# Kernel optimization log

Measured on AMD Instinct MI355X. Metric: run time of the kernel, lower is better.

## Reference

```python
import jax, jax.numpy as jnp
import numpy as np

B, F, E, V = 16384, 32, 16, 100000
D, S, K = 4, 8, 2            # domains, shared experts, specific experts per domain
I = F * E                    # input_dim = 512
OUT = 16
EPS = 1e-5


def _bn(x):
    # torch BatchNorm1d training mode: biased variance over batch
    m = jnp.mean(x, axis=0)
    v = jnp.var(x, axis=0)
    return (x - m) / jnp.sqrt(v + EPS)


def setup_inputs() -> dict:
    key = jax.random.key(0)
    ks = jax.random.split(key, 24)
    inp = {
        "ids": jax.random.randint(ks[0], (B, F), 0, V),
        "domain_id": jax.random.randint(ks[1], (B,), 0, D),
        "emb_table": jax.random.normal(ks[2], (F, V, E), jnp.float32) * 0.05,
        "domain_weight": jax.random.normal(ks[3], (D, I), jnp.float32) * 0.06,
        "domain_bias": jax.random.uniform(ks[4], (D, I), jnp.float32),
        # shared experts: BN affine + Linear(I->16)
        "sh_gamma": jnp.ones((S, I), jnp.float32),
        "sh_beta": jnp.zeros((S, I), jnp.float32),
        "sh_W": jax.random.normal(ks[5], (S, I, OUT), jnp.float32) * 0.04,
        "sh_b": jnp.zeros((S, OUT), jnp.float32),
        # domain-specific experts
        "sp_gamma": jnp.ones((D, K, I), jnp.float32),
        "sp_beta": jnp.zeros((D, K, I), jnp.float32),
        "sp_W": jax.random.normal(ks[6], (D, K, I, OUT), jnp.float32) * 0.04,
        "sp_b": jnp.zeros((D, K, OUT), jnp.float32),
        # gate
        "gate_W": jax.random.normal(ks[7], (I, S + K), jnp.float32) * 0.04,
        "gate_b": jnp.zeros((S + K,), jnp.float32),
        # final MLP 16 -> 32 -> 32 -> 1 (Linear+BN+ReLU per hidden layer)
        "mlp_W1": jax.random.normal(ks[8], (OUT, 32), jnp.float32) * 0.25,
        "mlp_b1": jnp.zeros((32,), jnp.float32),
        "mlp_g1": jnp.ones((32,), jnp.float32),
        "mlp_be1": jnp.zeros((32,), jnp.float32),
        "mlp_W2": jax.random.normal(ks[9], (32, 32), jnp.float32) * 0.18,
        "mlp_b2": jnp.zeros((32,), jnp.float32),
        "mlp_g2": jnp.ones((32,), jnp.float32),
        "mlp_be2": jnp.zeros((32,), jnp.float32),
        "mlp_W3": jax.random.normal(ks[10], (32, 1), jnp.float32) * 0.18,
        "mlp_b3": jnp.zeros((1,), jnp.float32),
    }
    return inp


def reference(ids, domain_id, emb_table, domain_weight, domain_bias,
              sh_gamma, sh_beta, sh_W, sh_b,
              sp_gamma, sp_beta, sp_W, sp_b,
              gate_W, gate_b,
              mlp_W1, mlp_b1, mlp_g1, mlp_be1,
              mlp_W2, mlp_b2, mlp_g2, mlp_be2,
              mlp_W3, mlp_b3):
    # embedding lookup: per-field table gather -> [B, F, E] -> [B, I]
    emb = emb_table[jnp.arange(F)[None, :], ids].reshape(B, I)

    # torch.where over domain masks collapses to a gather of per-domain affine
    shared_emb = emb * domain_weight[domain_id] + domain_bias[domain_id]  # [B, I]

    # shared experts: BN stats shared (same input), per-expert affine + linear
    xh = _bn(shared_emb)  # [B, I]
    shared_out = (jnp.einsum('bi,si,sio->bso', xh, sh_gamma, sh_W)
                  + (jnp.einsum('si,sio->so', sh_beta, sh_W) + sh_b)[None])  # [B, S, 16]

    # domain-specific experts run on the FULL batch per domain (dense dispatch)
    dom_in = emb[None] * domain_weight[:, None, :] + domain_bias[:, None, :]  # [D, B, I]
    xh_d = jax.vmap(_bn)(dom_in)  # [D, B, I]
    spec = (jnp.einsum('dbi,dki,dkio->dbko', xh_d, sp_gamma, sp_W)
            + (jnp.einsum('dki,dkio->dko', sp_beta, sp_W) + sp_b)[:, None])  # [D, B, K, 16]
    specific_emb = spec[domain_id, jnp.arange(B)]  # [B, K, 16] (masked select)

    expert_out = jnp.concatenate([shared_out, specific_emb], axis=1)  # [B, S+K, 16]
    gate = jax.nn.softmax(shared_emb @ gate_W + gate_b, axis=-1)       # [B, S+K]
    mix = jnp.sum(expert_out * gate[..., None], axis=1)               # [B, 16]

    h = jax.nn.relu(_bn(mix @ mlp_W1 + mlp_b1) * mlp_g1 + mlp_be1)
    h = jax.nn.relu(_bn(h @ mlp_W2 + mlp_b2) * mlp_g2 + mlp_be2)
    logit = (h @ mlp_W3 + mlp_b3)[:, 0]
    return jax.nn.sigmoid(logit)
```

## Files before the change

kernel.cpp:

```cpp
#include <hip/hip_runtime.h>
#include <hip/hip_bf16.h>

#define B_    16384
#define F_    32
#define E_    16
#define V_    100000
#define D_    4
#define S_    8
#define K_    2
#define I_    512
#define OUT_  16
#define SK_   10
#define C_    192
#define OSTR  193
#define EPS_  1e-5f
#define NG    16

typedef __attribute__((ext_vector_type(4))) float f32x4;
typedef __attribute__((ext_vector_type(8))) short bf16x8;

__device__ __forceinline__ unsigned short f2bf(float x) {
    unsigned u = __float_as_uint(x);
    unsigned r = (u + 0x7fffu + ((u >> 16) & 1u)) >> 16;
    return (unsigned short)r;
}

__global__ __launch_bounds__(512) void k_gather(
    const int* __restrict__ ids, const int* __restrict__ dom,
    const float* __restrict__ tbl, unsigned short* __restrict__ emb,
    float* __restrict__ S1G, float* __restrict__ S2G)
{
    const int t = threadIdx.x;
    const int slot = t & 127;
    const int rsub = t >> 7;
    const int f = slot >> 2;
    const int e0 = (slot & 3) << 2;
    const int rbase = blockIdx.x * 4 + rsub;
    const float* fbase = tbl + (size_t)f * V_ * E_ + e0;

    int idv[8];
#pragma unroll
    for (int it = 0; it < 8; ++it)
        idv[it] = ids[(rbase + it * 2048) * F_ + f];
    float4 v[8];
#pragma unroll
    for (int it = 0; it < 8; ++it)
        v[it] = *(const float4*)(fbase + (size_t)idv[it] * E_);
    int dv[8];
#pragma unroll
    for (int it = 0; it < 8; ++it)
        dv[it] = dom[rbase + it * 2048];

    float sa[4][4], qa[4][4];
#pragma unroll
    for (int d = 0; d < 4; ++d)
#pragma unroll
        for (int c = 0; c < 4; ++c) { sa[d][c] = 0.f; qa[d][c] = 0.f; }

#pragma unroll
    for (int it = 0; it < 8; ++it) {
        const int r = rbase + it * 2048;
        unsigned p0 = (unsigned)f2bf(v[it].x) | ((unsigned)f2bf(v[it].y) << 16);
        unsigned p1 = (unsigned)f2bf(v[it].z) | ((unsigned)f2bf(v[it].w) << 16);
        *(uint2*)(emb + (size_t)r * I_ + slot * 4) = make_uint2(p0, p1);
        const int d = dv[it];
#pragma unroll
        for (int dd = 0; dd < 4; ++dd) {
            const float m = (d == dd) ? 1.f : 0.f;
            sa[dd][0] = fmaf(m, v[it].x, sa[dd][0]); qa[dd][0] = fmaf(m * v[it].x, v[it].x, qa[dd][0]);
            sa[dd][1] = fmaf(m, v[it].y, sa[dd][1]); qa[dd][1] = fmaf(m * v[it].y, v[it].y, qa[dd][1]);
            sa[dd][2] = fmaf(m, v[it].z, sa[dd][2]); qa[dd][2] = fmaf(m * v[it].z, v[it].z, qa[dd][2]);
            sa[dd][3] = fmaf(m, v[it].w, sa[dd][3]); qa[dd][3] = fmaf(m * v[it].w, v[it].w, qa[dd][3]);
        }
    }

    __shared__ float red[2][128][36];
    if (rsub >= 2) {
        float* p = red[rsub - 2][slot];
#pragma unroll
        for (int d = 0; d < 4; ++d)
#pragma unroll
            for (int c = 0; c < 4; ++c) { p[d * 4 + c] = sa[d][c]; p[16 + d * 4 + c] = qa[d][c]; }
    }
    __syncthreads();
    if (rsub < 2) {
        float* p = red[rsub][slot];
#pragma unroll
        for (int d = 0; d < 4; ++d)
#pragma unroll
            for (int c = 0; c < 4; ++c) { sa[d][c] += p[d * 4 + c]; qa[d][c] += p[16 + d * 4 + c]; }
    }
    __syncthreads();
    if (rsub == 1) {
        float* p = red[0][slot];
#pragma unroll
        for (int d = 0; d < 4; ++d)
#pragma unroll
            for (int c = 0; c < 4; ++c) { p[d * 4 + c] = sa[d][c]; p[16 + d * 4 + c] = qa[d][c]; }
    }
    __syncthreads();
    if (rsub == 0) {
        float* p = red[0][slot];
        const int g = blockIdx.x & (NG - 1);
#pragma unroll
        for (int d = 0; d < 4; ++d)
#pragma unroll
            for (int c = 0; c < 4; ++c) {
                atomicAdd(&S1G[(g * 4 + d) * 512 + slot * 4 + c], sa[d][c] + p[d * 4 + c]);
                atomicAdd(&S2G[(g * 4 + d) * 512 + slot * 4 + c], qa[d][c] + p[16 + d * 4 + c]);
            }
    }
}

__global__ __launch_bounds__(256) void k_bucket(
    const int* __restrict__ dom, int* __restrict__ cnt, int* __restrict__ rl)
{
    const int t = threadIdx.x;
    const int r = blockIdx.x * 256 + t;
    const int d = dom[r];
    const int wv = t >> 6;
    const int lane = t & 63;
    __shared__ int wcnt[4][4];
    int myoff = 0;
#pragma unroll
    for (int dd = 0; dd < 4; ++dd) {
        unsigned long long m = __ballot(d == dd);
        if (lane == 0) wcnt[dd][wv] = (int)__popcll(m);
        if (d == dd) myoff = (int)__popcll(m & ((1ull << lane) - 1ull));
    }
    __syncthreads();
    if (t < 4) {
        int c0 = wcnt[t][0], c1 = wcnt[t][1], c2 = wcnt[t][2], c3 = wcnt[t][3];
        int b = atomicAdd(&cnt[t], c0 + c1 + c2 + c3);
        wcnt[t][0] = b; wcnt[t][1] = b + c0; wcnt[t][2] = b + c0 + c1; wcnt[t][3] = b + c0 + c1 + c2;
    }
    __syncthreads();
    rl[d * B_ + wcnt[d][wv] + myoff] = r;
}

__global__ __launch_bounds__(256) void k_stats(
    const float* __restrict__ S1G, const float* __restrict__ S2G, const int* __restrict__ cnt,
    const float* __restrict__ dw, const float* __restrict__ db,
    float* __restrict__ m_, float* __restrict__ dq, float* __restrict__ mu, float* __restrict__ isg)
{
    const int i = blockIdx.x * 256 + threadIdx.x;
    float nd[4], s1v[4], s2v[4], wv[4], bv[4];
#pragma unroll
    for (int d = 0; d < 4; ++d) {
        nd[d] = (float)cnt[d];
        float a = 0.f, b = 0.f;
#pragma unroll
        for (int g = 0; g < NG; ++g) {
            a += S1G[(g * 4 + d) * 512 + i];
            b += S2G[(g * 4 + d) * 512 + i];
        }
        s1v[d] = a; s2v[d] = b;
        wv[d] = dw[d * I_ + i];  bv[d] = db[d * I_ + i];
    }
    const float invB = 1.0f / (float)B_;
    float tot1 = s1v[0] + s1v[1] + s1v[2] + s1v[3];
    float tot2 = s2v[0] + s2v[1] + s2v[2] + s2v[3];
    float m = tot1 * invB;
    float v = fmaxf(tot2 * invB - m * m, 0.f);
    m_[i] = m;
#pragma unroll
    for (int d = 0; d < 4; ++d)
        dq[d * I_ + i] = wv[d] / sqrtf(v * wv[d] * wv[d] + EPS_);
    float ssum = 0.f, ssq = 0.f;
#pragma unroll
    for (int d = 0; d < 4; ++d) {
        ssum += wv[d] * s1v[d] + nd[d] * bv[d];
        ssq  += wv[d] * wv[d] * s2v[d] + 2.f * wv[d] * bv[d] * s1v[d] + nd[d] * bv[d] * bv[d];
    }
    float muv = ssum * invB;
    float var = fmaxf(ssq * invB - muv * muv, 0.f);
    mu[i] = muv;
    isg[i] = 1.f / sqrtf(var + EPS_);
}

__global__ __launch_bounds__(256) void k_fold(
    const float* __restrict__ dw, const float* __restrict__ isg, const float* __restrict__ dq,
    const float* __restrict__ shg, const float* __restrict__ shW,
    const float* __restrict__ spg, const float* __restrict__ spW,
    const float* __restrict__ gW, unsigned short* __restrict__ MB,
    const float* __restrict__ m_, const float* __restrict__ mu,
    const float* __restrict__ db,
    const float* __restrict__ shb_, const float* __restrict__ shb2,
    const float* __restrict__ spb_, const float* __restrict__ spb2,
    const float* __restrict__ gb, float* __restrict__ bias)
{
    const int d = blockIdx.y;
    const int t = threadIdx.x;
    if (blockIdx.x < 192) {
        const int ct = blockIdx.x >> 4, ic = blockIdx.x & 15;
        const int lane = t >> 2, jp = t & 3;
        const int c = ct * 16 + (lane & 15);
        unsigned short hi2[2], lo2[2];
#pragma unroll
        for (int jj = 0; jj < 2; ++jj) {
            const int i = ic * 32 + (lane >> 4) * 8 + jp * 2 + jj;
            float val = 0.f;
            if (c < 128) {
                const int s = c >> 4, o = c & 15;
                val = dw[d * I_ + i] * isg[i] * shg[s * I_ + i] * shW[((size_t)s * I_ + i) * OUT_ + o];
            } else if (c < 160) {
                const int k = (c - 128) >> 4, o = c & 15;
                val = dq[d * I_ + i] * spg[((size_t)(d * K_ + k)) * I_ + i]
                    * spW[(((size_t)(d * K_ + k)) * I_ + i) * OUT_ + o];
            } else if (c < 170) {
                val = dw[d * I_ + i] * gW[i * SK_ + (c - 160)];
            }
            unsigned short h = f2bf(val);
            float hv = __uint_as_float((unsigned)h << 16);
            hi2[jj] = h;
            lo2[jj] = f2bf(val - hv);
        }
        const size_t base = (((size_t)(d * 12 + ct) * 16 + ic) * 2) * 512 + lane * 8 + jp * 2;
        *(ushort2*)(MB + base)       = make_ushort2(hi2[0], hi2[1]);
        *(ushort2*)(MB + base + 512) = make_ushort2(lo2[0], lo2[1]);
        return;
    }
    const int e = blockIdx.x - 192;
    __shared__ float red[256][17];
    float acc[16];
#pragma unroll
    for (int o = 0; o < 16; ++o) acc[o] = 0.f;

    if (e < 8) {
        for (int i = t; i < I_; i += 256) {
            float coef = (db[d * I_ + i] - mu[i]) * isg[i] * shg[e * I_ + i] + shb_[e * I_ + i];
            const float* wp = &shW[((size_t)e * I_ + i) * OUT_];
#pragma unroll
            for (int o = 0; o < 16; ++o) acc[o] += coef * wp[o];
        }
    } else if (e < 10) {
        const int k = e - 8;
        for (int i = t; i < I_; i += 256) {
            float coef = -m_[i] * dq[d * I_ + i] * spg[((size_t)(d * K_ + k)) * I_ + i]
                       + spb_[((size_t)(d * K_ + k)) * I_ + i];
            const float* wp = &spW[(((size_t)(d * K_ + k)) * I_ + i) * OUT_];
#pragma unroll
            for (int o = 0; o < 16; ++o) acc[o] += coef * wp[o];
        }
    } else {
        for (int i = t; i < I_; i += 256) {
            float bb = db[d * I_ + i];
#pragma unroll
            for (int g = 0; g < 10; ++g) acc[g] += bb * gW[i * SK_ + g];
        }
    }
#pragma unroll
    for (int o = 0; o < 16; ++o) red[t][o] = acc[o];
    __syncthreads();
    for (int st = 128; st > 0; st >>= 1) {
        if (t < st) {
#pragma unroll
            for (int o = 0; o < 16; ++o) red[t][o] += red[t + st][o];
        }
        __syncthreads();
    }
    if (t == 0) {
        if (e < 8) {
            for (int o = 0; o < 16; ++o) bias[d * C_ + e * 16 + o] = red[0][o] + shb2[e * 16 + o];
        } else if (e < 10) {
            const int k = e - 8;
            for (int o = 0; o < 16; ++o)
                bias[d * C_ + 128 + k * 16 + o] = red[0][o] + spb2[(d * K_ + k) * 16 + o];
        } else {
            for (int g = 0; g < 10; ++g) bias[d * C_ + 160 + g] = red[0][g] + gb[g];
            for (int c = 170; c < C_; ++c) bias[d * C_ + c] = 0.f;
        }
    }
}

__global__ __launch_bounds__(512) void k_main(
    const unsigned short* __restrict__ emb, const int* __restrict__ rl, const int* __restrict__ cnt,
    const unsigned short* __restrict__ MB, const float* __restrict__ bias,
    const float* __restrict__ W1, const float* __restrict__ b1,
    float* __restrict__ h1g, float* __restrict__ h1s, float* __restrict__ h1q)
{
    const int d = blockIdx.y, tile = blockIdx.x;
    const int base = tile * 32;
    const int rem = cnt[d] - base;
    if (rem <= 0) return;
    const int nn = rem < 32 ? rem : 32;
    const int t = threadIdx.x;

    __shared__ int rid[32];
    __shared__ float smem[32 * OSTR + 32 * 33];
    float* obuf  = smem;
    float* h1buf = smem + 32 * OSTR;

    if (t < 32) rid[t] = rl[d * B_ + base + (t < nn ? t : nn - 1)];
    __syncthreads();

    const int wv = t >> 6, lane = t & 63;
    const int rt = wv & 1, ch = wv >> 1;
    const int l15 = lane & 15, lk = lane >> 4;

    const unsigned short* arow  = emb + (size_t)rid[rt * 16 + l15] * I_ + lk * 8;
    const unsigned short* bbase = MB + (size_t)d * 196608 + (size_t)(ch * 3) * 16384 + lane * 8;

    f32x4 acc[3];
#pragma unroll
    for (int c3 = 0; c3 < 3; ++c3) acc[c3] = (f32x4){0.f, 0.f, 0.f, 0.f};

#pragma unroll 4
    for (int ic = 0; ic < 16; ++ic) {
        const bf16x8 a = *(const bf16x8*)(arow + ic * 32);
#pragma unroll
        for (int c3 = 0; c3 < 3; ++c3) {
            const unsigned short* bp = bbase + (size_t)c3 * 16384 + ic * 1024;
            const bf16x8 bh = *(const bf16x8*)bp;
            const bf16x8 bl = *(const bf16x8*)(bp + 512);
            acc[c3] = __builtin_amdgcn_mfma_f32_16x16x32_bf16(a, bh, acc[c3], 0, 0, 0);
            acc[c3] = __builtin_amdgcn_mfma_f32_16x16x32_bf16(a, bl, acc[c3], 0, 0, 0);
        }
    }

    const float* bd = bias + d * C_;
#pragma unroll
    for (int c3 = 0; c3 < 3; ++c3) {
        const int col = ch * 48 + c3 * 16 + l15;
        const float bv = bd[col];
#pragma unroll
        for (int j = 0; j < 4; ++j) {
            const int row = rt * 16 + lk * 4 + j;
            obuf[row * OSTR + col] = acc[c3][j] + bv;
        }
    }
    __syncthreads();

    if (t < 32) {
        const float* row = &obuf[t * OSTR];
        float g[10];
        float mx = row[160];
#pragma unroll
        for (int e = 1; e < 10; ++e) mx = fmaxf(mx, row[160 + e]);
        float ssum = 0.f;
#pragma unroll
        for (int e = 0; e < 10; ++e) { g[e] = __expf(row[160 + e] - mx); ssum += g[e]; }
        const float inv = 1.f / ssum;
        float mix[16];
#pragma unroll
        for (int o = 0; o < 16; ++o) mix[o] = 0.f;
#pragma unroll
        for (int e = 0; e < 10; ++e) {
#pragma unroll
            for (int o = 0; o < 16; ++o) mix[o] = fmaf(g[e], row[e * 16 + o], mix[o]);
        }
#pragma unroll
        for (int o = 0; o < 16; ++o) mix[o] *= inv;
#pragma unroll
        for (int o2 = 0; o2 < 32; ++o2) {
            float a = b1[o2];
#pragma unroll
            for (int o = 0; o < 16; ++o) a = fmaf(mix[o], W1[o * 32 + o2], a);
            h1buf[t * 33 + o2] = a;
        }
    }
    __syncthreads();
    if (t < 32) {
        float s = 0.f, q = 0.f;
        for (int r = 0; r < nn; ++r) { float v = h1buf[r * 33 + t]; s += v; q += v * v; }
        const int g = (blockIdx.x + blockIdx.y) & (NG - 1);
        atomicAdd(&h1s[g * 32 + t], s); atomicAdd(&h1q[g * 32 + t], q);
    }
#pragma unroll
    for (int k = 0; k < 2; ++k) {
        const int idx = k * 512 + t;
        const int r = idx >> 5, c = idx & 31;
        if (r < nn) h1g[(size_t)rid[r] * 32 + c] = h1buf[r * 33 + c];
    }
}

__global__ __launch_bounds__(256) void k_mlp1(
    const float* __restrict__ h1g, const float* __restrict__ s1, const float* __restrict__ s2,
    const float* __restrict__ g1, const float* __restrict__ be1,
    const float* __restrict__ W2, const float* __restrict__ b2,
    float* __restrict__ h2g, float* __restrict__ h2s, float* __restrict__ h2q)
{
    __shared__ float hb[64 * 33];
    __shared__ float ab[64 * 33];
    __shared__ float w2t[32 * 32];
    __shared__ float scl[32], shf[32];
    const int t = threadIdx.x;
    const size_t rb = (size_t)blockIdx.x * 64;
#pragma unroll
    for (int k = 0; k < 2; ++k) {
        const int w = k * 1024 + t * 4;
        const int r = w >> 5, c = w & 31;
        *(float4*)&hb[r * 33 + c] = *(const float4*)&h1g[rb * 32 + w];
    }
#pragma unroll
    for (int k = 0; k < 4; ++k) {
        const int idx = k * 256 + t;
        const int i = idx >> 5, o = idx & 31;
        w2t[o * 32 + i] = W2[idx];
    }
    if (t < 32) {
        float s = 0.f, q = 0.f;
#pragma unroll
        for (int g = 0; g < NG; ++g) { s += s1[g * 32 + t]; q += s2[g * 32 + t]; }
        const float invB = 1.0f / (float)B_;
        float mn = s * invB;
        float vr = fmaxf(q * invB - mn * mn, 0.f);
        float iv = 1.f / sqrtf(vr + EPS_);
        scl[t] = iv * g1[t]; shf[t] = be1[t] - mn * iv * g1[t];
    }
    __syncthreads();
    const int r = t >> 2, sub = t & 3;
#pragma unroll
    for (int k = 0; k < 8; ++k) {
        const int i = sub * 8 + k;
        float x = hb[r * 33 + i] * scl[i] + shf[i];
        ab[r * 33 + i] = fmaxf(x, 0.f);
    }
    __syncthreads();
    float h2[8];
#pragma unroll
    for (int kk = 0; kk < 8; ++kk) {
        const int o = sub * 8 + kk;
        float acc = b2[o];
#pragma unroll
        for (int i = 0; i < 32; i += 4) {
            const float4 w4 = *(const float4*)&w2t[o * 32 + i];
            acc = fmaf(ab[r * 33 + i], w4.x, acc);
            acc = fmaf(ab[r * 33 + i + 1], w4.y, acc);
            acc = fmaf(ab[r * 33 + i + 2], w4.z, acc);
            acc = fmaf(ab[r * 33 + i + 3], w4.w, acc);
        }
        h2[kk] = acc;
    }
    __syncthreads();
#pragma unroll
    for (int kk = 0; kk < 8; ++kk) hb[r * 33 + sub * 8 + kk] = h2[kk];
    __syncthreads();
    if (t < 32) {
        float s = 0.f, q = 0.f;
        for (int rr = 0; rr < 64; ++rr) { float v = hb[rr * 33 + t]; s += v; q += v * v; }
        const int g = blockIdx.x & (NG - 1);
        atomicAdd(&h2s[g * 32 + t], s); atomicAdd(&h2q[g * 32 + t], q);
    }
#pragma unroll
    for (int k = 0; k < 2; ++k) {
        const int w = k * 1024 + t * 4;
        const int r2 = w >> 5, c = w & 31;
        *(float4*)&h2g[rb * 32 + w] = *(const float4*)&hb[r2 * 33 + c];
    }
}

__global__ __launch_bounds__(256) void k_mlp2(
    const float* __restrict__ h2g, const float* __restrict__ s1, const float* __restrict__ s2,
    const float* __restrict__ g2, const float* __restrict__ be2,
    const float* __restrict__ W3, const float* __restrict__ b3, float* __restrict__ out)
{
    __shared__ float hb[64 * 33];
    __shared__ float scl[32], shf[32], w3s[32];
    const int t = threadIdx.x;
    const size_t rb = (size_t)blockIdx.x * 64;
#pragma unroll
    for (int k = 0; k < 2; ++k) {
        const int w = k * 1024 + t * 4;
        const int r = w >> 5, c = w & 31;
        *(float4*)&hb[r * 33 + c] = *(const float4*)&h2g[rb * 32 + w];
    }
    if (t < 32) {
        float s = 0.f, q = 0.f;
#pragma unroll
        for (int g = 0; g < NG; ++g) { s += s1[g * 32 + t]; q += s2[g * 32 + t]; }
        const float invB = 1.0f / (float)B_;
        float mn = s * invB;
        float vr = fmaxf(q * invB - mn * mn, 0.f);
        float iv = 1.f / sqrtf(vr + EPS_);
        scl[t] = iv * g2[t]; shf[t] = be2[t] - mn * iv * g2[t];
        w3s[t] = W3[t];
    }
    __syncthreads();
    if (t < 64) {
        float acc = b3[0];
#pragma unroll
        for (int i = 0; i < 32; ++i) {
            float x = hb[t * 33 + i] * scl[i] + shf[i];
            x = fmaxf(x, 0.f);
            acc = fmaf(x, w3s[i], acc);
        }
        out[rb + t] = 1.f / (1.f + __expf(-acc));
    }
}

extern "C" void kernel_launch(void* const* d_in, const int* in_sizes, int n_in,
                              void* d_out, int out_size, void* d_ws, size_t ws_size,
                              hipStream_t stream) {
    const int*   ids  = (const int*)d_in[0];
    const int*   dom  = (const int*)d_in[1];
    const float* tbl  = (const float*)d_in[2];
    const float* dw   = (const float*)d_in[3];
    const float* db   = (const float*)d_in[4];
    const float* shg  = (const float*)d_in[5];
    const float* shb_ = (const float*)d_in[6];
    const float* shW  = (const float*)d_in[7];
    const float* shb2 = (const float*)d_in[8];
    const float* spg  = (const float*)d_in[9];
    const float* spb_ = (const float*)d_in[10];
    const float* spW  = (const float*)d_in[11];
    const float* spb2 = (const float*)d_in[12];
    const float* gW   = (const float*)d_in[13];
    const float* gb   = (const float*)d_in[14];
    const float* W1   = (const float*)d_in[15];
    const float* b1   = (const float*)d_in[16];
    const float* g1   = (const float*)d_in[17];
    const float* be1  = (const float*)d_in[18];
    const float* W2   = (const float*)d_in[19];
    const float* b2   = (const float*)d_in[20];
    const float* g2   = (const float*)d_in[21];
    const float* be2  = (const float*)d_in[22];
    const float* W3   = (const float*)d_in[23];
    const float* b3   = (const float*)d_in[24];
    float* out = (float*)d_out;

    float* ws = (float*)d_ws;
    float* S1G  = ws + 0;
    float* S2G  = ws + 32768;
    float* H1S  = ws + 65536;
    float* H1Q  = ws + 66048;
    float* H2S  = ws + 66560;
    float* H2Q  = ws + 67072;
    int*   CNT  = (int*)(ws + 67584);
    float* M0v  = ws + 67600;
    float* DQ   = ws + 68112;
    float* MU   = ws + 70160;
    float* ISG  = ws + 70672;
    float* BIASW= ws + 71184;
    unsigned short* MB = (unsigned short*)(ws + 71952);
    int*   RL   = (int*)(ws + 465168);
    unsigned short* EMB = (unsigned short*)(ws + 530704);
    float* H1G  = ws + 4725008;
    float* H2G  = ws + 5249296;

    hipMemsetAsync(d_ws, 0, 270400, stream);

    k_gather<<<512, 512, 0, stream>>>(ids, dom, tbl, EMB, S1G, S2G);
    k_bucket<<<64, 256, 0, stream>>>(dom, CNT, RL);
    k_stats<<<2, 256, 0, stream>>>(S1G, S2G, CNT, dw, db, M0v, DQ, MU, ISG);
    k_fold<<<dim3(203, 4), 256, 0, stream>>>(dw, ISG, DQ, shg, shW, spg, spW, gW, MB,
                                             M0v, MU, db, shb_, shb2, spb_, spb2, gb, BIASW);
    k_main<<<dim3(512, 4), 512, 0, stream>>>(EMB, RL, CNT, MB, BIASW, W1, b1, H1G, H1S, H1Q);
    k_mlp1<<<256, 256, 0, stream>>>(H1G, H1S, H1Q, g1, be1, W2, b2, H2G, H2S, H2Q);
    k_mlp2<<<256, 256, 0, stream>>>(H2G, H2S, H2Q, g2, be2, W3, b3, out);
}
```

Measured before the change: 383.0 us.

## Fuse domain bucketing into gather, widen stat atomic groups, parallelize gate mix

Domain bucketing (count plus row list) moves into the gather kernel, which removes one launch. Each block counts its 32 rows through shared memory and reserves slots with atomics. The number of atomic partial-sum groups for the embedding stats doubles to 32 to reduce atomic contention, which means a larger memset and a longer reduction loop in k_stats. In k_main, the gate-weighted mix and the W1 projection are spread across all threads through shared buffers, with W1 and b1 staged in LDS, instead of 32 threads doing them serially. Row order inside each domain bucket changes, which alters summation order but not results beyond rounding.

```diff
diff --git a/kernel.cpp b/kernel.cpp
--- a/kernel.cpp
+++ b/kernel.cpp
@@ -14,7 +14,8 @@
 #define C_    192
 #define OSTR  193
 #define EPS_  1e-5f
-#define NG    16
+#define NG    32
+#define NGH   16
 
 typedef __attribute__((ext_vector_type(4))) float f32x4;
 typedef __attribute__((ext_vector_type(8))) short bf16x8;
@@ -28,7 +29,8 @@
 __global__ __launch_bounds__(512) void k_gather(
     const int* __restrict__ ids, const int* __restrict__ dom,
     const float* __restrict__ tbl, unsigned short* __restrict__ emb,
-    float* __restrict__ S1G, float* __restrict__ S2G)
+    float* __restrict__ S1G, float* __restrict__ S2G,
+    int* __restrict__ cnt, int* __restrict__ rl)
 {
     const int t = threadIdx.x;
     const int slot = t & 127;
@@ -38,6 +40,10 @@
     const int rbase = blockIdx.x * 4 + rsub;
     const float* fbase = tbl + (size_t)f * V_ * E_ + e0;
 
+    __shared__ int dombuf[32];
+    __shared__ int dbase[4];
+    __shared__ float red[2][128][36];
+
     int idv[8];
 #pragma unroll
     for (int it = 0; it < 8; ++it)
@@ -50,6 +56,11 @@
 #pragma unroll
     for (int it = 0; it < 8; ++it)
         dv[it] = dom[rbase + it * 2048];
+
+    if (slot == 0) {
+#pragma unroll
+        for (int it = 0; it < 8; ++it) dombuf[rsub * 8 + it] = dv[it];
+    }
 
     float sa[4][4], qa[4][4];
 #pragma unroll
@@ -74,7 +85,6 @@
         }
     }
 
-    __shared__ float red[2][128][36];
     if (rsub >= 2) {
         float* p = red[rsub - 2][slot];
 #pragma unroll
@@ -110,32 +120,20 @@
                 atomicAdd(&S2G[(g * 4 + d) * 512 + slot * 4 + c], qa[d][c] + p[16 + d * 4 + c]);
             }
     }
-}
-
-__global__ __launch_bounds__(256) void k_bucket(
-    const int* __restrict__ dom, int* __restrict__ cnt, int* __restrict__ rl)
-{
-    const int t = threadIdx.x;
-    const int r = blockIdx.x * 256 + t;
-    const int d = dom[r];
-    const int wv = t >> 6;
-    const int lane = t & 63;
-    __shared__ int wcnt[4][4];
-    int myoff = 0;
-#pragma unroll
-    for (int dd = 0; dd < 4; ++dd) {
-        unsigned long long m = __ballot(d == dd);
-        if (lane == 0) wcnt[dd][wv] = (int)__popcll(m);
-        if (d == dd) myoff = (int)__popcll(m & ((1ull << lane) - 1ull));
-    }
-    __syncthreads();
     if (t < 4) {
-        int c0 = wcnt[t][0], c1 = wcnt[t][1], c2 = wcnt[t][2], c3 = wcnt[t][3];
-        int b = atomicAdd(&cnt[t], c0 + c1 + c2 + c3);
-        wcnt[t][0] = b; wcnt[t][1] = b + c0; wcnt[t][2] = b + c0 + c1; wcnt[t][3] = b + c0 + c1 + c2;
-    }
-    __syncthreads();
-    rl[d * B_ + wcnt[d][wv] + myoff] = r;
+        int count = 0;
+#pragma unroll
+        for (int j = 0; j < 32; ++j) count += (dombuf[j] == t);
+        dbase[t] = atomicAdd(&cnt[t], count);
+    }
+    __syncthreads();
+    if (t < 32) {
+        const int d = dombuf[t];
+        int pref = 0;
+        for (int j = 0; j < t; ++j) pref += (dombuf[j] == d);
+        const int row = blockIdx.x * 4 + (t >> 3) + (t & 7) * 2048;
+        rl[d * B_ + dbase[d] + pref] = row;
+    }
 }
 
 __global__ __launch_bounds__(256) void k_stats(
@@ -149,7 +147,6 @@
     for (int d = 0; d < 4; ++d) {
         nd[d] = (float)cnt[d];
         float a = 0.f, b = 0.f;
-#pragma unroll
         for (int g = 0; g < NG; ++g) {
             a += S1G[(g * 4 + d) * 512 + i];
             b += S2G[(g * 4 + d) * 512 + i];
@@ -287,11 +284,16 @@
     const int t = threadIdx.x;
 
     __shared__ int rid[32];
-    __shared__ float smem[32 * OSTR + 32 * 33];
-    float* obuf  = smem;
-    float* h1buf = smem + 32 * OSTR;
+    __shared__ float obuf[32 * OSTR];
+    __shared__ float h1buf[32 * 33];
+    __shared__ float gbuf[32][11];
+    __shared__ float mixbuf[32 * 17];
+    __shared__ float w1s[512];
+    __shared__ float b1s[32];
 
     if (t < 32) rid[t] = rl[d * B_ + base + (t < nn ? t : nn - 1)];
+    w1s[t] = W1[t];
+    if (t < 32) b1s[t] = b1[t];
     __syncthreads();
 
     const int wv = t >> 6, lane = t & 63;
@@ -341,29 +343,34 @@
 #pragma unroll
         for (int e = 0; e < 10; ++e) { g[e] = __expf(row[160 + e] - mx); ssum += g[e]; }
         const float inv = 1.f / ssum;
-        float mix[16];
-#pragma unroll
-        for (int o = 0; o < 16; ++o) mix[o] = 0.f;
-#pragma unroll
-        for (int e = 0; e < 10; ++e) {
-#pragma unroll
-            for (int o = 0; o < 16; ++o) mix[o] = fmaf(g[e], row[e * 16 + o], mix[o]);
-        }
-#pragma unroll
-        for (int o = 0; o < 16; ++o) mix[o] *= inv;
-#pragma unroll
-        for (int o2 = 0; o2 < 32; ++o2) {
-            float a = b1[o2];
-#pragma unroll
-            for (int o = 0; o < 16; ++o) a = fmaf(mix[o], W1[o * 32 + o2], a);
-            h1buf[t * 33 + o2] = a;
-        }
+#pragma unroll
+        for (int e = 0; e < 10; ++e) gbuf[t][e] = g[e] * inv;
+    }
+    __syncthreads();
+    {
+        const int row = t >> 4, o = t & 15;
+        const float* rp = &obuf[row * OSTR + o];
+        float m = 0.f;
+#pragma unroll
+        for (int e = 0; e < 10; ++e) m = fmaf(gbuf[row][e], rp[e * 16], m);
+        mixbuf[row * 17 + o] = m;
+    }
+    __syncthreads();
+#pragma unroll
+    for (int k = 0; k < 2; ++k) {
+        const int idx = k * 512 + t;
+        const int row = idx >> 5, o2 = idx & 31;
+        float a = b1s[o2];
+        const float* mp = &mixbuf[row * 17];
+#pragma unroll
+        for (int o = 0; o < 16; ++o) a = fmaf(mp[o], w1s[o * 32 + o2], a);
+        h1buf[row * 33 + o2] = a;
     }
     __syncthreads();
     if (t < 32) {
         float s = 0.f, q = 0.f;
         for (int r = 0; r < nn; ++r) { float v = h1buf[r * 33 + t]; s += v; q += v * v; }
-        const int g = (blockIdx.x + blockIdx.y) & (NG - 1);
+        const int g = (blockIdx.x + blockIdx.y) & (NGH - 1);
         atomicAdd(&h1s[g * 32 + t], s); atomicAdd(&h1q[g * 32 + t], q);
     }
 #pragma unroll
@@ -401,7 +408,7 @@
     if (t < 32) {
         float s = 0.f, q = 0.f;
 #pragma unroll
-        for (int g = 0; g < NG; ++g) { s += s1[g * 32 + t]; q += s2[g * 32 + t]; }
+        for (int g = 0; g < NGH; ++g) { s += s1[g * 32 + t]; q += s2[g * 32 + t]; }
         const float invB = 1.0f / (float)B_;
         float mn = s * invB;
         float vr = fmaxf(q * invB - mn * mn, 0.f);
@@ -439,7 +446,7 @@
     if (t < 32) {
         float s = 0.f, q = 0.f;
         for (int rr = 0; rr < 64; ++rr) { float v = hb[rr * 33 + t]; s += v; q += v * v; }
-        const int g = blockIdx.x & (NG - 1);
+        const int g = blockIdx.x & (NGH - 1);
         atomicAdd(&h2s[g * 32 + t], s); atomicAdd(&h2q[g * 32 + t], q);
     }
 #pragma unroll
@@ -468,7 +475,7 @@
     if (t < 32) {
         float s = 0.f, q = 0.f;
 #pragma unroll
-        for (int g = 0; g < NG; ++g) { s += s1[g * 32 + t]; q += s2[g * 32 + t]; }
+        for (int g = 0; g < NGH; ++g) { s += s1[g * 32 + t]; q += s2[g * 32 + t]; }
         const float invB = 1.0f / (float)B_;
         float mn = s * invB;
         float vr = fmaxf(q * invB - mn * mn, 0.f);
@@ -521,27 +528,26 @@
 
     float* ws = (float*)d_ws;
     float* S1G  = ws + 0;
-    float* S2G  = ws + 32768;
-    float* H1S  = ws + 65536;
-    float* H1Q  = ws + 66048;
-    float* H2S  = ws + 66560;
-    float* H2Q  = ws + 67072;
-    int*   CNT  = (int*)(ws + 67584);
-    float* M0v  = ws + 67600;
-    float* DQ   = ws + 68112;
-    float* MU   = ws + 70160;
-    float* ISG  = ws + 70672;
-    float* BIASW= ws + 71184;
-    unsigned short* MB = (unsigned short*)(ws + 71952);
-    int*   RL   = (int*)(ws + 465168);
-    unsigned short* EMB = (unsigned short*)(ws + 530704);
-    float* H1G  = ws + 4725008;
-    float* H2G  = ws + 5249296;
-
-    hipMemsetAsync(d_ws, 0, 270400, stream);
-
-    k_gather<<<512, 512, 0, stream>>>(ids, dom, tbl, EMB, S1G, S2G);
-    k_bucket<<<64, 256, 0, stream>>>(dom, CNT, RL);
+    float* S2G  = ws + 65536;
+    float* H1S  = ws + 131072;
+    float* H1Q  = ws + 131584;
+    float* H2S  = ws + 132096;
+    float* H2Q  = ws + 132608;
+    int*   CNT  = (int*)(ws + 133120);
+    float* M0v  = ws + 133136;
+    float* DQ   = ws + 133648;
+    float* MU   = ws + 135696;
+    float* ISG  = ws + 136208;
+    float* BIASW= ws + 136720;
+    unsigned short* MB = (unsigned short*)(ws + 137488);
+    int*   RL   = (int*)(ws + 530704);
+    unsigned short* EMB = (unsigned short*)(ws + 596240);
+    float* H1G  = ws + 4790544;
+    float* H2G  = ws + 5314832;
+
+    hipMemsetAsync(d_ws, 0, 532496, stream);
+
+    k_gather<<<512, 512, 0, stream>>>(ids, dom, tbl, EMB, S1G, S2G, CNT, RL);
     k_stats<<<2, 256, 0, stream>>>(S1G, S2G, CNT, dw, db, M0v, DQ, MU, ISG);
     k_fold<<<dim3(203, 4), 256, 0, stream>>>(dw, ISG, DQ, shg, shW, spg, spW, gW, MB,
                                              M0v, MU, db, shb_, shb2, spb_, spb2, gb, BIASW);
```

Result: no change. 390.1 us (+1.9%).
